# Optimization experiments

Hardware: AMD Instinct MI355X
Metric: run time of the kernel (lower is better)

The kernel has to match this reference:

```python
import jax, jax.numpy as jnp
import numpy as np
from jax import lax

B, C, D, H, W = 4, 256, 32, 32, 32
LATENT = 512


def setup_inputs() -> dict:
    key = jax.random.key(0)
    k = jax.random.split(key, 6)
    x = jax.random.normal(k[0], (B, C, D, H, W), dtype=jnp.float32)
    prev_rgb = jax.random.normal(k[1], (B, 1, D, H, W), dtype=jnp.float32)
    istyle = jax.random.normal(k[2], (B, LATENT), dtype=jnp.float32)
    # nn.Linear(latent_dim, input_channel): weight [C, LATENT], bias [C]
    lim = 1.0 / np.sqrt(LATENT)
    W_style = jax.random.uniform(k[3], (C, LATENT), minval=-lim, maxval=lim, dtype=jnp.float32)
    b_style = jax.random.uniform(k[4], (C,), minval=-lim, maxval=lim, dtype=jnp.float32)
    # Conv3DMod weight [out=1, C, 1,1,1], kaiming_normal fan_in, leaky_relu(a=0) gain=sqrt(2)
    conv_weight = jax.random.normal(k[5], (1, C, 1, 1, 1), dtype=jnp.float32) * np.float32(np.sqrt(2.0 / C))
    return {"x": x, "prev_rgb": prev_rgb, "istyle": istyle,
            "W_style": W_style, "b_style": b_style, "conv_weight": conv_weight}


def _blur3d(x):
    # kornia filter3d with normalized 3x3x3 [1,2,1] outer-product kernel, replicate padding
    f = jnp.array([1.0, 2.0, 1.0], dtype=x.dtype)
    ker = f[:, None, None] * f[None, :, None] * f[None, None, :]
    ker = (ker / ker.sum())[None, None]  # [1,1,3,3,3] (single channel)
    xp = jnp.pad(x, ((0, 0), (0, 0), (1, 1), (1, 1), (1, 1)), mode='edge')
    return lax.conv_general_dilated(
        xp, ker, window_strides=(1, 1, 1), padding='VALID',
        dimension_numbers=('NCDHW', 'OIDHW', 'NCDHW'))


def reference(x, prev_rgb, istyle, W_style, b_style, conv_weight):
    b, c, d, h, w = x.shape
    # to_style linear
    style = istyle @ W_style.T + b_style                    # [b, c]
    # Conv3DMod, kernel=1, demod=False: per-sample modulated weights reduce to a
    # per-(sample, channel) coefficient; conv is a channel-weighted sum.
    wk = conv_weight[0, :, 0, 0, 0]                         # [c]
    coef = wk[None, :] * (style + 1.0)                      # [b, c]
    out = jnp.einsum('bcdhw,bc->bdhw', x, coef)[:, None]    # [b,1,d,h,w]
    out = out + prev_rgb
    # Upsample scale=2, trilinear, align_corners=False (half-pixel centers)
    out = jax.image.resize(out, (b, 1, 2 * d, 2 * h, 2 * w), method='trilinear')
    out = _blur3d(out)
    return out
```

## Files before the change

kernel.cpp:

```cpp
#include <hip/hip_runtime.h>

#define BATCH 4
#define CH    256
#define SVOL  32768
#define SV4   8192
#define TILE  64
#define NCH   4
#define CCH   64

typedef float floatx4 __attribute__((ext_vector_type(4)));


__global__ void __launch_bounds__(256)
coef_kernel(const float* __restrict__ istyle,
            const float* __restrict__ W_style,
            const float* __restrict__ b_style,
            const float* __restrict__ wk,
            float* __restrict__ coef) {
    int tid  = threadIdx.x;
    int wave = blockIdx.x * 4 + (tid >> 6);
    int lane = tid & 63;
    int b = wave >> 8;
    int c = wave & 255;
    const float* is = istyle + b * 512;
    const float* wr = W_style + c * 512;
    float acc = 0.f;
    #pragma unroll
    for (int j = 0; j < 8; ++j) {
        int k = lane + j * 64;
        acc += is[k] * wr[k];
    }
    #pragma unroll
    for (int off = 32; off >= 1; off >>= 1)
        acc += __shfl_down(acc, off, 64);
    if (lane == 0)
        coef[b * 256 + c] = wk[c] * (acc + b_style[c] + 1.0f);
}

__global__ void __launch_bounds__(256)
reduce_c_kernel(const floatx4* __restrict__ x4,
                const float* __restrict__ coef,
                const floatx4* __restrict__ prev4,
                floatx4* __restrict__ small4) {
    __shared__ float   cf[CH];
    __shared__ floatx4 red[NCH][TILE];

    int t     = threadIdx.x;
    int pos   = t & (TILE - 1);
    int chunk = t >> 6;
    int gpos  = blockIdx.x * TILE + pos;
    int b     = gpos >> 13;
    int s4    = gpos & (SV4 - 1);

    cf[t] = coef[b * CH + t];
    __syncthreads();

    const floatx4* xp = x4 + (size_t)(b * CH + chunk * CCH) * SV4 + s4;
    const float*   cw = &cf[chunk * CCH];

    floatx4 acc0 = {0.f, 0.f, 0.f, 0.f};
    floatx4 acc1 = {0.f, 0.f, 0.f, 0.f};
    #pragma unroll 8
    for (int cc = 0; cc < CCH; cc += 2) {
        floatx4 v0 = xp[(size_t)cc * SV4];
        floatx4 v1 = xp[(size_t)(cc + 1) * SV4];
        acc0 += v0 * cw[cc];
        acc1 += v1 * cw[cc + 1];
    }
    red[chunk][pos] = acc0 + acc1;
    __syncthreads();

    if (t < TILE) {
        floatx4 r = prev4[gpos];
        #pragma unroll
        for (int k = 0; k < NCH; ++k)
            r += red[k][t];
        small4[gpos] = r;
    }
}

__global__ void __launch_bounds__(256)
upblur_kernel(const float* __restrict__ small,
              float* __restrict__ out) {
    int g  = blockIdx.x * 256 + threadIdx.x;
    int xo = g & 63;
    int yo = (g >> 6) & 63;
    int zo = (g >> 12) & 63;
    int b  = g >> 18;

    int jx = xo >> 1, jy = yo >> 1, jz = zo >> 1;
    int px = xo & 1,  py = yo & 1,  pz = zo & 1;

    int xi[3] = { jx > 0 ? jx - 1 : 0, jx, jx < 31 ? jx + 1 : 31 };
    int yi[3] = { jy > 0 ? jy - 1 : 0, jy, jy < 31 ? jy + 1 : 31 };
    int zi[3] = { jz > 0 ? jz - 1 : 0, jz, jz < 31 ? jz + 1 : 31 };

    float wx[3] = { px ? 1.f : 5.f, 10.f, px ? 5.f : 1.f };
    float wy[3] = { py ? 1.f : 5.f, 10.f, py ? 5.f : 1.f };
    float wz[3] = { pz ? 1.f : 5.f, 10.f, pz ? 5.f : 1.f };

    const float* base = small + (size_t)b * SVOL;
    float acc = 0.f;
    #pragma unroll
    for (int a = 0; a < 3; ++a) {
        const float* pzrow = base + zi[a] * 1024;
        float accy = 0.f;
        #pragma unroll
        for (int c = 0; c < 3; ++c) {
            const float* pyrow = pzrow + yi[c] * 32;
            float row = wx[0] * pyrow[xi[0]] + wx[1] * pyrow[xi[1]] + wx[2] * pyrow[xi[2]];
            accy += wy[c] * row;
        }
        acc += wz[a] * accy;
    }
    out[g] = acc * (1.0f / 4096.0f);
}

extern "C" void kernel_launch(void* const* d_in, const int* in_sizes, int n_in,
                              void* d_out, int out_size, void* d_ws, size_t ws_size,
                              hipStream_t stream) {
    const float* x       = (const float*)d_in[0];
    const float* prev    = (const float*)d_in[1];
    const float* istyle  = (const float*)d_in[2];
    const float* W_style = (const float*)d_in[3];
    const float* b_style = (const float*)d_in[4];
    const float* wk      = (const float*)d_in[5];
    float* ws    = (float*)d_ws;
    float* coef  = ws;
    float* small = ws + 1024;

    coef_kernel<<<256, 256, 0, stream>>>(istyle, W_style, b_style, wk, coef);

    reduce_c_kernel<<<BATCH * SV4 / TILE, 256, 0, stream>>>(
        (const floatx4*)x, coef, (const floatx4*)prev, (floatx4*)small);

    upblur_kernel<<<BATCH * 64 * 64 * 64 / 256, 256, 0, stream>>>(small, (float*)d_out);
}
```

Measured before the change: 207.8 us.

## Retile channel reduction, use nontemporal loads, vectorize upsample-blur output

The channel-reduction kernel now splits 256 channels into 8 chunks of 32 over 32-position tiles, which doubles the block count, and reads x with nontemporal loads to avoid polluting cache with streamed data. The upsample+blur kernel now has each thread compute four adjacent x outputs from four shared input samples and store them as one float4. This cuts redundant loads and index math and gives wider stores. The trade-off is a larger shared reduction step and possibly less per-thread load parallelism in the reduction.

```diff
diff --git a/kernel.cpp b/kernel.cpp
--- a/kernel.cpp
+++ b/kernel.cpp
@@ -4,9 +4,9 @@
 #define CH    256
 #define SVOL  32768
 #define SV4   8192
-#define TILE  64
-#define NCH   4
-#define CCH   64
+#define TILE  32
+#define NCH   8
+#define CCH   32
 
 typedef float floatx4 __attribute__((ext_vector_type(4)));
 
@@ -47,7 +47,7 @@
 
     int t     = threadIdx.x;
     int pos   = t & (TILE - 1);
-    int chunk = t >> 6;
+    int chunk = t >> 5;
     int gpos  = blockIdx.x * TILE + pos;
     int b     = gpos >> 13;
     int s4    = gpos & (SV4 - 1);
@@ -62,8 +62,8 @@
     floatx4 acc1 = {0.f, 0.f, 0.f, 0.f};
     #pragma unroll 8
     for (int cc = 0; cc < CCH; cc += 2) {
-        floatx4 v0 = xp[(size_t)cc * SV4];
-        floatx4 v1 = xp[(size_t)(cc + 1) * SV4];
+        floatx4 v0 = __builtin_nontemporal_load(&xp[(size_t)cc * SV4]);
+        floatx4 v1 = __builtin_nontemporal_load(&xp[(size_t)(cc + 1) * SV4]);
         acc0 += v0 * cw[cc];
         acc1 += v1 * cw[cc + 1];
     }
@@ -81,39 +81,45 @@
 
 __global__ void __launch_bounds__(256)
 upblur_kernel(const float* __restrict__ small,
-              float* __restrict__ out) {
-    int g  = blockIdx.x * 256 + threadIdx.x;
-    int xo = g & 63;
-    int yo = (g >> 6) & 63;
-    int zo = (g >> 12) & 63;
-    int b  = g >> 18;
+              floatx4* __restrict__ out4) {
+    int g4 = blockIdx.x * 256 + threadIdx.x;
+    int u  = g4 & 15;
+    int yo = (g4 >> 4) & 63;
+    int zo = (g4 >> 10) & 63;
+    int b  = g4 >> 16;
 
-    int jx = xo >> 1, jy = yo >> 1, jz = zo >> 1;
-    int px = xo & 1,  py = yo & 1,  pz = zo & 1;
+    int jy = yo >> 1, jz = zo >> 1;
+    int py = yo & 1,  pz = zo & 1;
 
-    int xi[3] = { jx > 0 ? jx - 1 : 0, jx, jx < 31 ? jx + 1 : 31 };
     int yi[3] = { jy > 0 ? jy - 1 : 0, jy, jy < 31 ? jy + 1 : 31 };
     int zi[3] = { jz > 0 ? jz - 1 : 0, jz, jz < 31 ? jz + 1 : 31 };
-
-    float wx[3] = { px ? 1.f : 5.f, 10.f, px ? 5.f : 1.f };
     float wy[3] = { py ? 1.f : 5.f, 10.f, py ? 5.f : 1.f };
     float wz[3] = { pz ? 1.f : 5.f, 10.f, pz ? 5.f : 1.f };
 
+    int xa = 2 * u - 1; if (xa < 0) xa = 0;
+    int xb = 2 * u;
+    int xc = 2 * u + 1;
+    int xd = 2 * u + 2; if (xd > 31) xd = 31;
+
     const float* base = small + (size_t)b * SVOL;
-    float acc = 0.f;
+    floatx4 acc = {0.f, 0.f, 0.f, 0.f};
     #pragma unroll
     for (int a = 0; a < 3; ++a) {
-        const float* pzrow = base + zi[a] * 1024;
-        float accy = 0.f;
+        const float* zrow = base + zi[a] * 1024;
+        floatx4 accy = {0.f, 0.f, 0.f, 0.f};
         #pragma unroll
         for (int c = 0; c < 3; ++c) {
-            const float* pyrow = pzrow + yi[c] * 32;
-            float row = wx[0] * pyrow[xi[0]] + wx[1] * pyrow[xi[1]] + wx[2] * pyrow[xi[2]];
-            accy += wy[c] * row;
+            const float* yrow = zrow + yi[c] * 32;
+            float ra = yrow[xa], rb = yrow[xb], rc = yrow[xc], rd = yrow[xd];
+            floatx4 rr = { 5.f * ra + 10.f * rb + rc,
+                           ra + 10.f * rb + 5.f * rc,
+                           5.f * rb + 10.f * rc + rd,
+                           rb + 10.f * rc + 5.f * rd };
+            accy += wy[c] * rr;
         }
         acc += wz[a] * accy;
     }
-    out[g] = acc * (1.0f / 4096.0f);
+    out4[g4] = acc * (1.0f / 4096.0f);
 }
 
 extern "C" void kernel_launch(void* const* d_in, const int* in_sizes, int n_in,
@@ -134,5 +140,6 @@
     reduce_c_kernel<<<BATCH * SV4 / TILE, 256, 0, stream>>>(
         (const floatx4*)x, coef, (const floatx4*)prev, (floatx4*)small);
 
-    upblur_kernel<<<BATCH * 64 * 64 * 64 / 256, 256, 0, stream>>>(small, (float*)d_out);
+    upblur_kernel<<<BATCH * 64 * 64 * 16 / 256, 256, 0, stream>>>(
+        small, (floatx4*)d_out);
 }
```

After: 196.3 us. -5.6%, faster.
